# Optimization experiments

Measured on AMD Instinct MI355X. Metric: run time of the kernel, lower is better.

Reference implementation:

```python
import jax, jax.numpy as jnp
import numpy as np

B, S, HID = 2, 2048, 2048
NH, NKV, D = 16, 8, 128      # heads, kv heads, head_dim
G = NH // NKV                # kv groups = 2
THETA = 1000000.0


def setup_inputs() -> dict:
    key = jax.random.key(0)
    ks = jax.random.split(key, 8)
    std = 0.02
    return {
        "hidden_states": jax.random.normal(ks[0], (B, S, HID), dtype=jnp.float32),
        "Wq": jax.random.normal(ks[1], (HID, NH * D), dtype=jnp.float32) * std,
        "bq": jax.random.normal(ks[2], (NH * D,), dtype=jnp.float32) * std,
        "Wk": jax.random.normal(ks[3], (HID, NKV * D), dtype=jnp.float32) * std,
        "bk": jax.random.normal(ks[4], (NKV * D,), dtype=jnp.float32) * std,
        "Wv": jax.random.normal(ks[5], (HID, NKV * D), dtype=jnp.float32) * std,
        "bv": jax.random.normal(ks[6], (NKV * D,), dtype=jnp.float32) * std,
        "Wo": jax.random.normal(ks[7], (NH * D, HID), dtype=jnp.float32) * std,
    }


def _rope_tables(seq_len, dim, dtype):
    # freqs: [dim/2]; emb = cat([ang, ang], -1) as in the torch RotaryEmbedding
    freqs = 1.0 / (THETA ** (jnp.arange(0, dim, 2, dtype=jnp.float32) / dim))
    t = jnp.arange(seq_len, dtype=jnp.float32)
    ang = jnp.outer(t, freqs)                       # [S, D/2]
    emb = jnp.concatenate([ang, ang], axis=-1)      # [S, D]
    return jnp.cos(emb).astype(dtype), jnp.sin(emb).astype(dtype)


def _rotate_half(x):
    x1, x2 = x[..., : x.shape[-1] // 2], x[..., x.shape[-1] // 2:]
    return jnp.concatenate([-x2, x1], axis=-1)


def reference(hidden_states, Wq, bq, Wk, bk, Wv, bv, Wo):
    bs, s, _ = hidden_states.shape
    q = (hidden_states @ Wq + bq).reshape(bs, s, NH, D).transpose(0, 2, 1, 3)   # [B,NH,S,D]
    k = (hidden_states @ Wk + bk).reshape(bs, s, NKV, D).transpose(0, 2, 1, 3)  # [B,NKV,S,D]
    v = (hidden_states @ Wv + bv).reshape(bs, s, NKV, D).transpose(0, 2, 1, 3)

    cos, sin = _rope_tables(s, D, q.dtype)          # [S,D] each, broadcast over B,H
    q = q * cos + _rotate_half(q) * sin
    k = k * cos + _rotate_half(k) * sin

    # GQA without materializing repeated KV: group q heads by kv head
    qg = q.reshape(bs, NKV, G, s, D)
    scale = jnp.asarray(np.sqrt(D), q.dtype)
    scores = jnp.einsum('bkgsd,bktd->bkgst', qg, k) / scale  # [B,NKV,G,S,S]

    causal = jnp.tril(jnp.ones((s, s), dtype=bool))
    scores = jnp.where(causal, scores, jnp.asarray(-1e9, scores.dtype))

    probs = jax.nn.softmax(scores.astype(jnp.float32), axis=-1).astype(q.dtype)
    ctx = jnp.einsum('bkgst,bktd->bkgsd', probs, v)          # [B,NKV,G,S,D]
    ctx = ctx.reshape(bs, NH, s, D).transpose(0, 2, 1, 3).reshape(bs, s, NH * D)
    return ctx @ Wo
```

## Files before the change

kernel.cpp:

```cpp
#include <hip/hip_runtime.h>

typedef __bf16 bf16;
typedef __attribute__((ext_vector_type(8))) __bf16 bf16x8;
typedef __attribute__((ext_vector_type(4))) float f32x4;

constexpr int kS   = 2048;
constexpr int kNH  = 16;
constexpr int kNKV = 8;
constexpr int kD   = 128;
constexpr int kNqkv = 4096;

__device__ __forceinline__ void async_copy16(void* lds_base_uniform, const void* g) {
  __builtin_amdgcn_global_load_lds(
      (const __attribute__((address_space(1))) void*)g,
      (__attribute__((address_space(3))) void*)lds_base_uniform, 16, 0, 0);
}

__global__ void detect_dtype(const unsigned short* __restrict__ hs, int* __restrict__ flag) {
  __shared__ int cnt;
  if (threadIdx.x == 0) cnt = 0;
  __syncthreads();
  int local = 0;
  for (int i = threadIdx.x; i < 8192; i += 256) {
    int e = (hs[i] >> 7) & 0xFF;
    local += (e >= 0x85) ? 1 : 0;
  }
  atomicAdd(&cnt, local);
  __syncthreads();
  if (threadIdx.x == 0) flag[0] = (cnt > 256) ? 1 : 0;
}

__device__ __forceinline__ float ld_elem(const void* p, size_t i, int f32) {
  return f32 ? ((const float*)p)[i] : (float)((const bf16*)p)[i];
}

__device__ __forceinline__ bf16x8 load8(const void* base, size_t eoff, int f32) {
  if (f32) {
    const float* p = (const float*)base + eoff;
    f32x4 a = *(const f32x4*)p;
    f32x4 b = *(const f32x4*)(p + 4);
    bf16x8 r;
    r[0]=(bf16)a[0]; r[1]=(bf16)a[1]; r[2]=(bf16)a[2]; r[3]=(bf16)a[3];
    r[4]=(bf16)b[0]; r[5]=(bf16)b[1]; r[6]=(bf16)b[2]; r[7]=(bf16)b[3];
    return r;
  }
  return *(const bf16x8*)((const bf16*)base + eoff);
}

__global__ void convert_hs(const void* __restrict__ hs, bf16* __restrict__ out,
                           const int* __restrict__ flagp) {
  const int f32 = flagp[0];
  const size_t i = ((size_t)blockIdx.x * 256 + threadIdx.x) * 8;
  *(bf16x8*)(out + i) = load8(hs, i, f32);
}

__global__ void transpose_weights(const void* __restrict__ Wq, const void* __restrict__ Wk,
                                  const void* __restrict__ Wv, const void* __restrict__ Wo,
                                  bf16* __restrict__ WQKVT, bf16* __restrict__ WOT,
                                  const int* __restrict__ flagp, int zbase) {
  __shared__ bf16 tb[64][65];
  const int f32 = flagp[0];
  const int which = blockIdx.z + zbase;
  const void* src; bf16* dst; int N; int nbase;
  if      (which == 0) { src = Wq; dst = WQKVT; N = 2048; nbase = 0;    }
  else if (which == 1) { src = Wk; dst = WQKVT; N = 1024; nbase = 2048; }
  else if (which == 2) { src = Wv; dst = WQKVT; N = 1024; nbase = 3072; }
  else                 { src = Wo; dst = WOT;   N = 2048; nbase = 0;    }
  const int n0 = blockIdx.x * 64;
  if (n0 >= N) return;
  const int k0 = blockIdx.y * 64;
  const int tx = threadIdx.x & 63, ty = threadIdx.x >> 6;
#pragma unroll
  for (int i = 0; i < 16; ++i) {
    int ks = ty + 4*i;
    tb[ks][tx] = (bf16)ld_elem(src, (size_t)(k0 + ks) * N + n0 + tx, f32);
  }
  __syncthreads();
#pragma unroll
  for (int i = 0; i < 16; ++i) {
    int ns = ty + 4*i;
    dst[(size_t)(nbase + n0 + ns) * 2048 + k0 + tx] = tb[tx][ns];
  }
}

__global__ void concat_bias(const void* __restrict__ bq, const void* __restrict__ bk,
                            const void* __restrict__ bv, bf16* __restrict__ bias,
                            const int* __restrict__ flagp) {
  const int f32 = flagp[0];
  int i = blockIdx.x * 256 + threadIdx.x;
  float v;
  if (i < 2048)      v = ld_elem(bq, i, f32);
  else if (i < 3072) v = ld_elem(bk, i - 2048, f32);
  else               v = ld_elem(bv, i - 3072, f32);
  bias[i] = (bf16)v;
}

template<int BM>
__global__ __launch_bounds__(512, 1) void gemm_big_kernel(
    const bf16* __restrict__ A, const bf16* __restrict__ BT,
    const bf16* __restrict__ bias, void* __restrict__ C, int N, int K,
    const int* __restrict__ flagp, int c_ext, int mlog) {
  constexpr int RW = BM / 2;
  constexpr int AL = BM / 128;
  constexpr int ACN = RW / 16;
  constexpr int SLOT = BM * 64 + 16384;
  extern __shared__ bf16 lds[];
  const int cfl = c_ext ? flagp[0] : 0;
  const int t = threadIdx.x, lane = t & 63, wv = t >> 6;
  const int wm = wv >> 2, wn = wv & 3;
  const int quad = lane >> 4, l16 = lane & 15;

  const int f   = blockIdx.y * gridDim.x + blockIdx.x;
  const int tot = gridDim.x * gridDim.y;
  const int w   = (f & 7) * (tot >> 3) + (f >> 3);
  const int mb  = w & ((1 << mlog) - 1);
  const int nb  = w >> mlog;
  const int m0 = mb * BM, n0 = nb * 256;
  const int NT = K >> 6;

  const int soff = (l16 >> 1) * 64 + ((((l16 & 1) * 4 + quad) ^ (l16 >> 1)) * 8);

  const int grow = t >> 2, gch = t & 3;

  f32x4 zero = {0.f, 0.f, 0.f, 0.f};
  f32x4 acc[ACN][4];
#pragma unroll
  for (int i = 0; i < ACN; ++i)
#pragma unroll
    for (int j = 0; j < 4; ++j) acc[i][j] = zero;

  f32x4 raX[AL], rbX[2], raY[AL], rbY[2];

  auto gload = [&](int kt, int ks, f32x4* ra, f32x4* rb) {
    const size_t ko = (size_t)kt * 64 + ks * 32 + gch * 8;
#pragma unroll
    for (int q = 0; q < AL; ++q)
      ra[q] = *(const f32x4*)(A + (size_t)(m0 + q * 128 + grow) * K + ko);
#pragma unroll
    for (int q = 0; q < 2; ++q)
      rb[q] = *(const f32x4*)(BT + (size_t)(n0 + q * 128 + grow) * K + ko);
  };
  auto swrite = [&](int buf, int ks, const f32x4* ra, const f32x4* rb) {
    bf16* Au = lds + (size_t)buf * SLOT + ks * (BM * 32);
    bf16* Bu = lds + (size_t)buf * SLOT + BM * 64 + ks * 8192;
#pragma unroll
    for (int q = 0; q < AL; ++q) {
      const int r = q * 128 + grow, line = r >> 1;
      const int s = ((r & 1) * 4 + gch) ^ (line & 7);
      *(f32x4*)(Au + line * 64 + s * 8) = ra[q];
    }
#pragma unroll
    for (int q = 0; q < 2; ++q) {
      const int r = q * 128 + grow, line = r >> 1;
      const int s = ((r & 1) * 4 + gch) ^ (line & 7);
      *(f32x4*)(Bu + line * 64 + s * 8) = rb[q];
    }
  };

  gload(0, 0, raX, rbX); swrite(0, 0, raX, rbX);
  gload(0, 1, raX, rbX); swrite(0, 1, raX, rbX);
  gload((NT > 1) ? 1 : 0, 0, raY, rbY);
  asm volatile("s_waitcnt lgkmcnt(0)" ::: "memory");
  __builtin_amdgcn_s_barrier();

  for (int jt = 0; jt < NT; ++jt) {
    const int cur = jt & 1;
    const bf16* Abase = lds + (size_t)cur * SLOT;
    const bf16* Bbase = Abase + BM * 64;

    {
      bf16x8 af[ACN], bfr[4];
#pragma unroll
      for (int mi = 0; mi < ACN; ++mi)
        af[mi] = *(const bf16x8*)(Abase + (wm * RW + mi * 16) * 32 + soff);
#pragma unroll
      for (int ni = 0; ni < 4; ++ni)
        bfr[ni] = *(const bf16x8*)(Bbase + (wn * 64 + ni * 16) * 32 + soff);

      gload((jt + 1 < NT) ? jt + 1 : 0, 1, raX, rbX);
      swrite(1 - cur, 0, raY, rbY);

      asm volatile("s_waitcnt lgkmcnt(0)" ::: "memory");
      __builtin_amdgcn_s_barrier();
      __builtin_amdgcn_s_setprio(1);
#pragma unroll
      for (int mi = 0; mi < ACN; ++mi)
#pragma unroll
        for (int ni = 0; ni < 4; ++ni)
          acc[mi][ni] = __builtin_amdgcn_mfma_f32_16x16x32_bf16(
              af[mi], bfr[ni], acc[mi][ni], 0, 0, 0);
      __builtin_amdgcn_s_setprio(0);
    }

    {
      const bf16* Au = Abase + BM * 32;
      const bf16* Bu = Bbase + 8192;
      bf16x8 af[ACN], bfr[4];
#pragma unroll
      for (int mi = 0; mi < ACN; ++mi)
        af[mi] = *(const bf16x8*)(Au + (wm * RW + mi * 16) * 32 + soff);
#pragma unroll
      for (int ni = 0; ni < 4; ++ni)
        bfr[ni] = *(const bf16x8*)(Bu + (wn * 64 + ni * 16) * 32 + soff);

      gload((jt + 2 < NT) ? jt + 2 : 0, 0, raY, rbY);
      swrite(1 - cur, 1, raX, rbX);

      asm volatile("s_waitcnt lgkmcnt(0)" ::: "memory");
      __builtin_amdgcn_s_barrier();
      __builtin_amdgcn_s_setprio(1);
#pragma unroll
      for (int mi = 0; mi < ACN; ++mi)
#pragma unroll
        for (int ni = 0; ni < 4; ++ni)
          acc[mi][ni] = __builtin_amdgcn_mfma_f32_16x16x32_bf16(
              af[mi], bfr[ni], acc[mi][ni], 0, 0, 0);
      __builtin_amdgcn_s_setprio(0);
    }
  }

#pragma unroll
  for (int ni = 0; ni < 4; ++ni) {
    const int col = n0 + wn * 64 + ni * 16 + l16;
    const float bvf = bias ? (float)bias[col] : 0.0f;
#pragma unroll
    for (int mi = 0; mi < ACN; ++mi) {
      const int rowb = m0 + wm * RW + mi * 16 + quad * 4;
#pragma unroll
      for (int r = 0; r < 4; ++r) {
        const float v = acc[mi][ni][r] + bvf;
        const size_t idx = (size_t)(rowb + r) * N + col;
        if (cfl) ((float*)C)[idx] = v;
        else     ((bf16*)C)[idx]  = (bf16)v;
      }
    }
  }
}

__global__ void rope_kernel(bf16* __restrict__ C1) {
  const int tx = threadIdx.x & 63, ty = threadIdx.x >> 6;
  const int row = blockIdx.x * 4 + ty;
  const int hh = blockIdx.y;
  const int col = (hh < kNH) ? hh * kD : kNH*kD + (hh - kNH) * kD;
  const int s = row & (kS - 1);
  const float freq = __expf(-(float)tx * (13.815510557964274f / 64.0f));
  const float rev0 = (float)s * freq * 0.15915494309189535f;
  const float rev = rev0 - floorf(rev0);
  const float c  = __builtin_amdgcn_cosf(rev);
  const float sn = __builtin_amdgcn_sinf(rev);
  const size_t base = (size_t)row * kNqkv + col;
  const float x1 = (float)C1[base + tx];
  const float x2 = (float)C1[base + 64 + tx];
  C1[base + tx]      = (bf16)(x1 * c - x2 * sn);
  C1[base + 64 + tx] = (bf16)(x2 * c + x1 * sn);
}

__global__ void v_transpose(const bf16* __restrict__ C1, bf16* __restrict__ VT) {
  __shared__ bf16 tb[64][65];
  const int bkv = blockIdx.z;
  const int b = bkv >> 3, kv = bkv & 7;
  const int t0 = blockIdx.x * 64, d0 = blockIdx.y * 64;
  const int tx = threadIdx.x & 63, ty = threadIdx.x >> 6;
#pragma unroll
  for (int i = 0; i < 16; ++i) {
    int ts = ty + 4*i;
    tb[ts][tx] = C1[(size_t)(b*kS + t0 + ts) * kNqkv + 3072 + kv*kD + d0 + tx];
  }
  __syncthreads();
  const size_t obase = ((size_t)(b*kNKV + kv) * kD) * kS;
#pragma unroll
  for (int i = 0; i < 16; ++i) {
    int ds = ty + 4*i;
    VT[obase + (size_t)(d0 + ds) * kS + t0 + tx] = tb[tx][ds];
  }
}

__global__ __launch_bounds__(256) void attn_kernel(
    const bf16* __restrict__ C1, const bf16* __restrict__ VT, bf16* __restrict__ CTX) {
  constexpr int LDP = 72;
  __shared__ bf16 lds_k[2][64 * 128];
  __shared__ bf16 lds_v[2][128 * 64];
  __shared__ bf16 lds_p[4][16 * LDP];
  const int f = (blockIdx.z * gridDim.y + blockIdx.y) * gridDim.x + blockIdx.x;
  const int w = (f & 7) * 64 + (f >> 3);
  const int p = w & 15;
  const int rest = w >> 4;
  const int h = rest & 15;
  const int b = rest >> 4;
  const int qtA = 31 - p;
  const int qtB = p;
  const int kvh = h >> 1;
  const int t = threadIdx.x, lane = t & 63, wv = t >> 6;
  const int quad = lane >> 4, l16 = lane & 15;
  const float SC2 = 0.08838834764831845f * 1.4426950408889634f;

  bf16x8 qfA[4], qfB[4];
  {
    const size_t rowQA = (size_t)(b*kS + qtA*64 + wv*16 + l16) * kNqkv + h * kD;
    const size_t rowQB = (size_t)(b*kS + qtB*64 + wv*16 + l16) * kNqkv + h * kD;
#pragma unroll
    for (int c = 0; c < 4; ++c) {
      qfA[c] = *(const bf16x8*)(C1 + rowQA + c*32 + quad*8);
      qfB[c] = *(const bf16x8*)(C1 + rowQB + c*32 + quad*8);
    }
  }

  float lA[4] = {0,0,0,0}, lB[4] = {0,0,0,0};
  f32x4 oA[8], oB[8];
  f32x4 zero = {0.f, 0.f, 0.f, 0.f};
#pragma unroll
  for (int n = 0; n < 8; ++n) { oA[n] = zero; oB[n] = zero; }

  const int qrowA = qtA*64 + wv*16 + quad*4;
  const int qrowB = qtB*64 + wv*16 + quad*4;
  bf16* pw = &lds_p[wv][0];

  const size_t kbase = (size_t)b * kS * kNqkv + 2048 + kvh * kD;
  const size_t vbase = ((size_t)(b*kNKV + kvh) * kD) * kS;
  const int jv = (lane & 7) ^ ((lane >> 3) & 7);

  auto stage = [&](int buf, int k0) {
#pragma unroll
    for (int s2 = 0; s2 < 4; ++s2) {
      const int r = wv + s2 * 4;
      const int krow = r*4 + (lane >> 4);
      const int jk = (lane & 15) ^ (krow & 7);
      async_copy16(&lds_k[buf][r * 512], C1 + kbase + (size_t)(k0 + krow) * kNqkv + jk * 8);
      const int vrow = r*8 + (lane >> 3);
      async_copy16(&lds_v[buf][r * 512], VT + vbase + (size_t)vrow * kS + k0 + jv * 8);
    }
  };

  auto compute = [&](const bf16* kb_, const bf16* vb_, const bf16x8* qf,
                     f32x4* o_acc, float* l_acc, int qrow_base, int k0, bool diag) {
    f32x4 sc4[4];
    __builtin_amdgcn_s_setprio(1);
#pragma unroll
    for (int g = 0; g < 4; ++g) {
      f32x4 s_acc = zero;
#pragma unroll
      for (int c = 0; c < 4; ++c) {
        bf16x8 kf = *(const bf16x8*)(kb_ + (g*16 + l16) * 128 + (((c*4 + quad) ^ (l16 & 7)) * 8));
        s_acc = __builtin_amdgcn_mfma_f32_16x16x32_bf16(qf[c], kf, s_acc, 0, 0, 0);
      }
      sc4[g] = s_acc;
    }
    __builtin_amdgcn_s_setprio(0);
#pragma unroll
    for (int g = 0; g < 4; ++g) {
#pragma unroll
      for (int r = 0; r < 4; ++r) {
        float pv = __builtin_amdgcn_exp2f(fmaf(sc4[g][r], SC2, -24.f));
        if (diag && (k0 + g*16 + l16 > qrow_base + r)) pv = 0.f;
        l_acc[r] += pv;
        pw[(quad*4 + r) * LDP + g*16 + l16] = (bf16)pv;
      }
    }
    __builtin_amdgcn_wave_barrier();
    __builtin_amdgcn_s_setprio(1);
#pragma unroll
    for (int kk = 0; kk < 2; ++kk) {
      bf16x8 pf = *(const bf16x8*)(pw + l16 * LDP + kk*32 + quad*8);
#pragma unroll
      for (int n = 0; n < 8; ++n) {
        bf16x8 vf = *(const bf16x8*)(vb_ + (n*16 + l16) * 64 + (((kk*4 + quad) ^ (l16 & 7)) * 8));
        o_acc[n] = __builtin_amdgcn_mfma_f32_16x16x32_bf16(pf, vf, o_acc[n], 0, 0, 0);
      }
    }
    __builtin_amdgcn_s_setprio(0);
    __builtin_amdgcn_wave_barrier();
  };

  stage(0, 0);
  for (int kt = 0; kt <= qtA; ++kt) {
    const int cur = kt & 1;
    __syncthreads();
    if (kt + 1 <= qtA) stage(1 - cur, (kt + 1) * 64);
    const int k0 = kt * 64;
    compute(&lds_k[cur][0], &lds_v[cur][0], qfA, oA, lA, qrowA, k0, kt == qtA);
    if (kt <= qtB)
      compute(&lds_k[cur][0], &lds_v[cur][0], qfB, oB, lB, qrowB, k0, kt == qtB);
  }

  float invA[4], invB[4];
#pragma unroll
  for (int r = 0; r < 4; ++r) {
    float la = lA[r], lb = lB[r];
    la += __shfl_xor(la, 1); lb += __shfl_xor(lb, 1);
    la += __shfl_xor(la, 2); lb += __shfl_xor(lb, 2);
    la += __shfl_xor(la, 4); lb += __shfl_xor(lb, 4);
    la += __shfl_xor(la, 8); lb += __shfl_xor(lb, 8);
    invA[r] = 1.0f / la;     invB[r] = 1.0f / lb;
  }
#pragma unroll
  for (int n = 0; n < 8; ++n) {
#pragma unroll
    for (int r = 0; r < 4; ++r) {
      CTX[(size_t)(b*kS + qrowA + r) * (kNH*kD) + h*kD + n*16 + l16] = (bf16)(oA[n][r] * invA[r]);
      CTX[(size_t)(b*kS + qrowB + r) * (kNH*kD) + h*kD + n*16 + l16] = (bf16)(oB[n][r] * invB[r]);
    }
  }
}

extern "C" void kernel_launch(void* const* d_in, const int* in_sizes, int n_in,
                              void* d_out, int out_size, void* d_ws, size_t ws_size,
                              hipStream_t stream) {
  const void* hs = d_in[0];
  const void* Wq = d_in[1];
  const void* bq = d_in[2];
  const void* Wk = d_in[3];
  const void* bk = d_in[4];
  const void* Wv = d_in[5];
  const void* bv = d_in[6];
  const void* Wo = d_in[7];

  char* ws = (char*)d_ws;
  bf16* C1    = (bf16*)(ws + 0);
  bf16* WOT   = (bf16*)(ws + 0);
  bf16* WQKVT = (bf16*)(ws + 33554432);
  bf16* VT    = (bf16*)(ws + 33554432);
  bf16* CTX   = (bf16*)(ws + 41943040);
  bf16* HSB   = (bf16*)(ws + 58720256);
  bf16* BIAS  = (bf16*)(ws + 75497472);
  int*  FLAG  = (int*) (ws + 75505664);

  (void)hipFuncSetAttribute((const void*)gemm_big_kernel<256>,
                            hipFuncAttributeMaxDynamicSharedMemorySize, 131072);
  (void)hipFuncSetAttribute((const void*)gemm_big_kernel<128>,
                            hipFuncAttributeMaxDynamicSharedMemorySize, 98304);

  detect_dtype<<<1, 256, 0, stream>>>((const unsigned short*)hs, FLAG);
  convert_hs<<<4096, 256, 0, stream>>>(hs, HSB, FLAG);
  transpose_weights<<<dim3(32, 32, 3), 256, 0, stream>>>(Wq, Wk, Wv, Wo, WQKVT, WOT, FLAG, 0);
  concat_bias<<<16, 256, 0, stream>>>(bq, bk, bv, BIAS, FLAG);
  gemm_big_kernel<256><<<dim3(16, 16), 512, 131072, stream>>>(HSB, WQKVT, BIAS, C1, 4096, 2048, FLAG, 0, 4);
  rope_kernel<<<dim3(1024, 24), 256, 0, stream>>>(C1);
  v_transpose<<<dim3(32, 2, 16), 256, 0, stream>>>(C1, VT);
  attn_kernel<<<dim3(16, 16, 2), 256, 0, stream>>>(C1, VT, CTX);
  transpose_weights<<<dim3(32, 32, 1), 256, 0, stream>>>(Wq, Wk, Wv, Wo, WQKVT, WOT, FLAG, 3);
  gemm_big_kernel<128><<<dim3(8, 32), 512, 98304, stream>>>(CTX, WOT, nullptr, d_out, 2048, 2048, FLAG, 1, 5);
}
```

Measured before the change: 369.4 us.

## Restructure GEMM main loop into four-slot half-tile LDS ring pipeline

Replaces the double-buffered full-K-tile loop, which ran two unrolled halves, with a single loop over half-tiles (32-wide K steps). These rotate through four LDS slots, with one register staging set and one barrier per half-tile. The LDS write of the next half and the global load two steps ahead are issued before the MFMAs, and the barrier moves after compute so LDS writes overlap the MFMA work. Sched barriers pin the instruction ordering. The intent is to shrink register pressure and hide LDS write latency. The trade-off is a barrier placed differently and a global-load-to-LDS-write distance of only one step.

```diff
diff --git a/kernel.cpp b/kernel.cpp
--- a/kernel.cpp
+++ b/kernel.cpp
@@ -103,7 +103,7 @@
   constexpr int RW = BM / 2;
   constexpr int AL = BM / 128;
   constexpr int ACN = RW / 16;
-  constexpr int SLOT = BM * 64 + 16384;
+  constexpr int HALF = BM * 32 + 8192;
   extern __shared__ bf16 lds[];
   const int cfl = c_ext ? flagp[0] : 0;
   const int t = threadIdx.x, lane = t & 63, wv = t >> 6;
@@ -117,6 +117,7 @@
   const int nb  = w >> mlog;
   const int m0 = mb * BM, n0 = nb * 256;
   const int NT = K >> 6;
+  const int NP = NT * 2;
 
   const int soff = (l16 >> 1) * 64 + ((((l16 & 1) * 4 + quad) ^ (l16 >> 1)) * 8);
 
@@ -129,10 +130,11 @@
 #pragma unroll
     for (int j = 0; j < 4; ++j) acc[i][j] = zero;
 
-  f32x4 raX[AL], rbX[2], raY[AL], rbY[2];
-
-  auto gload = [&](int kt, int ks, f32x4* ra, f32x4* rb) {
-    const size_t ko = (size_t)kt * 64 + ks * 32 + gch * 8;
+  f32x4 ra[AL], rb[2];
+
+  auto gload = [&](int p) {
+    p = (p < NP) ? p : 0;
+    const size_t ko = (size_t)(p >> 1) * 64 + (p & 1) * 32 + gch * 8;
 #pragma unroll
     for (int q = 0; q < AL; ++q)
       ra[q] = *(const f32x4*)(A + (size_t)(m0 + q * 128 + grow) * K + ko);
@@ -140,9 +142,9 @@
     for (int q = 0; q < 2; ++q)
       rb[q] = *(const f32x4*)(BT + (size_t)(n0 + q * 128 + grow) * K + ko);
   };
-  auto swrite = [&](int buf, int ks, const f32x4* ra, const f32x4* rb) {
-    bf16* Au = lds + (size_t)buf * SLOT + ks * (BM * 32);
-    bf16* Bu = lds + (size_t)buf * SLOT + BM * 64 + ks * 8192;
+  auto swrite = [&](int p) {
+    bf16* Au = lds + (size_t)(p & 3) * HALF;
+    bf16* Bu = Au + BM * 32;
 #pragma unroll
     for (int q = 0; q < AL; ++q) {
       const int r = q * 128 + grow, line = r >> 1;
@@ -157,66 +159,38 @@
     }
   };
 
-  gload(0, 0, raX, rbX); swrite(0, 0, raX, rbX);
-  gload(0, 1, raX, rbX); swrite(0, 1, raX, rbX);
-  gload((NT > 1) ? 1 : 0, 0, raY, rbY);
+  gload(0); swrite(0);
+  gload(1);
   asm volatile("s_waitcnt lgkmcnt(0)" ::: "memory");
   __builtin_amdgcn_s_barrier();
-
-  for (int jt = 0; jt < NT; ++jt) {
-    const int cur = jt & 1;
-    const bf16* Abase = lds + (size_t)cur * SLOT;
-    const bf16* Bbase = Abase + BM * 64;
-
-    {
-      bf16x8 af[ACN], bfr[4];
-#pragma unroll
-      for (int mi = 0; mi < ACN; ++mi)
-        af[mi] = *(const bf16x8*)(Abase + (wm * RW + mi * 16) * 32 + soff);
+  __builtin_amdgcn_sched_barrier(0);
+
+  for (int p = 0; p < NP; ++p) {
+    const bf16* Au = lds + (size_t)(p & 3) * HALF;
+    const bf16* Bu = Au + BM * 32;
+    bf16x8 af[ACN], bfr[4];
+#pragma unroll
+    for (int mi = 0; mi < ACN; ++mi)
+      af[mi] = *(const bf16x8*)(Au + (wm * RW + mi * 16) * 32 + soff);
+#pragma unroll
+    for (int ni = 0; ni < 4; ++ni)
+      bfr[ni] = *(const bf16x8*)(Bu + (wn * 64 + ni * 16) * 32 + soff);
+
+    swrite(p + 1);
+    gload(p + 2);
+
+    __builtin_amdgcn_s_setprio(1);
+#pragma unroll
+    for (int mi = 0; mi < ACN; ++mi)
 #pragma unroll
       for (int ni = 0; ni < 4; ++ni)
-        bfr[ni] = *(const bf16x8*)(Bbase + (wn * 64 + ni * 16) * 32 + soff);
-
-      gload((jt + 1 < NT) ? jt + 1 : 0, 1, raX, rbX);
-      swrite(1 - cur, 0, raY, rbY);
-
-      asm volatile("s_waitcnt lgkmcnt(0)" ::: "memory");
-      __builtin_amdgcn_s_barrier();
-      __builtin_amdgcn_s_setprio(1);
-#pragma unroll
-      for (int mi = 0; mi < ACN; ++mi)
-#pragma unroll
-        for (int ni = 0; ni < 4; ++ni)
-          acc[mi][ni] = __builtin_amdgcn_mfma_f32_16x16x32_bf16(
-              af[mi], bfr[ni], acc[mi][ni], 0, 0, 0);
-      __builtin_amdgcn_s_setprio(0);
-    }
-
-    {
-      const bf16* Au = Abase + BM * 32;
-      const bf16* Bu = Bbase + 8192;
-      bf16x8 af[ACN], bfr[4];
-#pragma unroll
-      for (int mi = 0; mi < ACN; ++mi)
-        af[mi] = *(const bf16x8*)(Au + (wm * RW + mi * 16) * 32 + soff);
-#pragma unroll
-      for (int ni = 0; ni < 4; ++ni)
-        bfr[ni] = *(const bf16x8*)(Bu + (wn * 64 + ni * 16) * 32 + soff);
-
-      gload((jt + 2 < NT) ? jt + 2 : 0, 0, raY, rbY);
-      swrite(1 - cur, 1, raX, rbX);
-
-      asm volatile("s_waitcnt lgkmcnt(0)" ::: "memory");
-      __builtin_amdgcn_s_barrier();
-      __builtin_amdgcn_s_setprio(1);
-#pragma unroll
-      for (int mi = 0; mi < ACN; ++mi)
-#pragma unroll
-        for (int ni = 0; ni < 4; ++ni)
-          acc[mi][ni] = __builtin_amdgcn_mfma_f32_16x16x32_bf16(
-              af[mi], bfr[ni], acc[mi][ni], 0, 0, 0);
-      __builtin_amdgcn_s_setprio(0);
-    }
+        acc[mi][ni] = __builtin_amdgcn_mfma_f32_16x16x32_bf16(
+            af[mi], bfr[ni], acc[mi][ni], 0, 0, 0);
+    __builtin_amdgcn_s_setprio(0);
+
+    asm volatile("s_waitcnt lgkmcnt(0)" ::: "memory");
+    __builtin_amdgcn_s_barrier();
+    __builtin_amdgcn_sched_barrier(0);
   }
 
 #pragma unroll
```

Result: no change. 364.8 us (-1.3%).
